# Kernel tuning notes

Measured on AMD Instinct MI355X. Metric: run time of the kernel, lower is better.

## Reference

```python
import jax, jax.numpy as jnp
import numpy as np

# AnyPrecision bit-plane packing convention (documented, since the CUDA kernel's
# exact bit order is an implementation detail):
#  - qweight[b, o, w] is an int32 word holding bit-plane b for output channel o,
#    covering input features i = 32*w .. 32*w+31, LSB-first within the word.
#  - plane 0 is the least-significant bit of the w_bits-wide LUT index.
#  - dequantized weight[o, i] = lut[o, index(o, i)].

IN_FEATURES = 4096
OUT_FEATURES = 4096
MAX_BITS = 8
W_BITS = 4


def anyprec_dequant(qweight, lut, w_bits):
    """qweight: (max_bits, O, In//32) int32; lut: (O, 2**w_bits). Returns (O, In)."""
    O, W = qweight.shape[1], qweight.shape[2]
    shifts = jnp.arange(32, dtype=jnp.int32)  # LSB-first within each word
    # (w_bits, O, W, 32): bit of each weight at each plane
    bits = (qweight[:w_bits, :, :, None] >> shifts) & 1
    plane_weights = (jnp.int32(1) << jnp.arange(w_bits, dtype=jnp.int32))[:, None, None, None]
    idx = jnp.sum(bits * plane_weights, axis=0).reshape(O, W * 32)  # (O, In) LUT indices
    return jnp.take_along_axis(lut, idx, axis=1)  # (O, In)


def setup_inputs() -> dict:
    key = jax.random.key(0)
    k1, k2, k3, k4 = jax.random.split(key, 4)
    x = jax.random.normal(k1, (4, 2048, IN_FEATURES), dtype=jnp.float32)
    qweight = jax.random.randint(
        k2, (MAX_BITS, OUT_FEATURES, IN_FEATURES // 32), 0, 2147483647, dtype=jnp.int32)
    lut = jax.random.normal(k3, (OUT_FEATURES, 2 ** W_BITS), dtype=jnp.float32) * 0.05
    bias = jax.random.normal(k4, (OUT_FEATURES,), dtype=jnp.float32) * 0.02
    return {"x": x, "qweight": qweight, "lut": lut, "bias": bias, "w_bits": W_BITS}


def reference(x, qweight, lut, bias, w_bits):
    # GEMM path of AnyPrecisionLinear.forward (B*T > 1)
    weight = anyprec_dequant(qweight, lut, w_bits)         # (O, In)
    y = jnp.einsum('bti,oi->bto', x, weight)               # (B, T, O)
    return y + bias
```

## Files before the change

kernel.cpp:

```cpp
#include <hip/hip_runtime.h>
#include <hip/hip_bf16.h>
#include <stdint.h>

#define M_DIM 8192
#define N_DIM 4096
#define K_DIM 4096

typedef __attribute__((ext_vector_type(4))) float f32x4;
typedef __attribute__((ext_vector_type(4))) int   i32x4;

#define GLD_LDS16(gaddr, laddr)                                            \
  __builtin_amdgcn_global_load_lds(                                        \
      (const __attribute__((address_space(1))) uint32_t*)(gaddr),          \
      (__attribute__((address_space(3))) uint32_t*)(laddr), 16, 0, 0)


__global__ __launch_bounds__(256) void prep_kernel(
    const int* __restrict__ q, const float* __restrict__ lut,
    signed char* __restrict__ Wq, float* __restrict__ sw,
    const float* __restrict__ x, signed char* __restrict__ Xq,
    float* __restrict__ sxd) {
  __shared__ char sm[16384];
  const int b = blockIdx.x;
  const int tid = threadIdx.x;
  if (b < 2048) {
    const int ob = b >> 4, wb = b & 15;
    const int o_l = tid >> 3, w_l = tid & 7;
    const int o = ob * 32 + o_l;
    const int PLANE = N_DIM * (K_DIM / 32);
    const int base = o * (K_DIM / 32) + wb * 8 + w_l;
    uint32_t q0 = (uint32_t)q[base];
    uint32_t q1 = (uint32_t)q[PLANE + base];
    uint32_t q2 = (uint32_t)q[2 * PLANE + base];
    uint32_t q3 = (uint32_t)q[3 * PLANE + base];
    const float* lrow = lut + o * 16;
    float lmax = 1e-30f;
#pragma unroll
    for (int j = 0; j < 16; ++j) lmax = fmaxf(lmax, fabsf(lrow[j]));
    const float qs = 127.0f / lmax;
    signed char l8[16];
#pragma unroll
    for (int j = 0; j < 16; ++j)
      l8[j] = (signed char)(int)rintf(lrow[j] * qs);
    if (wb == 0 && w_l == 0) sw[o] = lmax * (1.0f / 127.0f);

    union { i32x4 v; signed char c[16]; } u0, u1;
#pragma unroll
    for (int i = 0; i < 16; ++i) {
      uint32_t idx = ((q0 >> i) & 1u) | (((q1 >> i) & 1u) << 1) |
                     (((q2 >> i) & 1u) << 2) | (((q3 >> i) & 1u) << 3);
      u0.c[i] = l8[idx];
    }
#pragma unroll
    for (int i = 16; i < 32; ++i) {
      uint32_t idx = ((q0 >> i) & 1u) | (((q1 >> i) & 1u) << 1) |
                     (((q2 >> i) & 1u) << 2) | (((q3 >> i) & 1u) << 3);
      u1.c[i - 16] = l8[idx];
    }
    const int t_local = w_l >> 1;
    const int f_local = o_l >> 4;
    const int kc0 = (w_l & 1) * 2;
    char* sp = sm + t_local * 2048 + f_local * 1024;
    *(i32x4*)(sp + ((o_l & 15) + kc0 * 16) * 16)       = u0.v;
    *(i32x4*)(sp + ((o_l & 15) + (kc0 + 1) * 16) * 16) = u1.v;
    __syncthreads();
    const int rp = ob >> 3, h = (ob >> 2) & 1, f0 = (ob * 2) & 7;
#pragma unroll
    for (int c = 0; c < 2; ++c) {
      const int ci = c * 256 + tid;
      const int t_loc = ci >> 7, off = ci & 127;
      const size_t outb = (size_t)(rp * 64 + wb * 4 + t_loc) * 16384
                          + h * 8192 + f0 * 1024 + off * 16;
      *(i32x4*)(Wq + outb) = *(i32x4*)(sm + t_loc * 2048 + off * 16);
    }
  } else {
    const int r = b - 2048;
    const float* xr = x + (size_t)r * K_DIM;
    float v[16];
#pragma unroll
    for (int s = 0; s < 4; ++s) {
      f32x4 u = *(const f32x4*)(xr + tid * 4 + s * 1024);
      v[s * 4 + 0] = u[0]; v[s * 4 + 1] = u[1];
      v[s * 4 + 2] = u[2]; v[s * 4 + 3] = u[3];
    }
    float m = 0.0f;
#pragma unroll
    for (int i = 0; i < 16; ++i) m = fmaxf(m, fabsf(v[i]));
#pragma unroll
    for (int off = 32; off; off >>= 1) m = fmaxf(m, __shfl_down(m, off));
    float* red = (float*)(sm + 8192);
    if ((tid & 63) == 0) red[tid >> 6] = m;
    __syncthreads();
    float rmax = fmaxf(fmaxf(red[0], red[1]), fmaxf(red[2], red[3]));
    rmax = fmaxf(rmax, 1e-30f);
    if (tid == 0) sxd[r] = rmax * (1.0f / 127.0f);
    const float qs = 127.0f / rmax;
#pragma unroll
    for (int s = 0; s < 4; ++s) {
      int qi[4];
#pragma unroll
      for (int j = 0; j < 4; ++j) {
        float qc = fminf(127.0f, fmaxf(-127.0f, rintf(v[s * 4 + j] * qs)));
        qi[j] = (int)qc;
      }
      uint32_t w = (qi[0] & 255) | ((qi[1] & 255) << 8) |
                   ((qi[2] & 255) << 16) | ((uint32_t)(qi[3] & 255) << 24);
      *(uint32_t*)(sm + tid * 4 + s * 1024) = w;
    }
    __syncthreads();
    const int rp = r >> 8, h = (r >> 7) & 1, f = (r >> 4) & 7;
    const int kt = tid >> 2, kc = tid & 3;
    const size_t outb = (size_t)(rp * 64 + kt) * 16384 + h * 8192
                        + f * 1024 + ((r & 15) + kc * 16) * 16;
    *(i32x4*)(Xq + outb) = *(i32x4*)(sm + tid * 16);
  }
}

__global__ __launch_bounds__(512, 2) void anyprec_gemm_kernel(
    const signed char* __restrict__ A,
    const signed char* __restrict__ B,
    const float* __restrict__ sxd, const float* __restrict__ sw,
    const float* __restrict__ bias,
    float* __restrict__ C) {
  __shared__ char lds[2][2][2][8192];

  int bid = blockIdx.x;
  int swz = (bid & 7) * 64 + (bid >> 3);
  int mb = swz >> 4;
  int nb = swz & 15;

  const int tid  = threadIdx.x;
  const int lane = tid & 63;
  const int wid  = tid >> 6;
  const int wr   = wid >> 2;
  const int wc   = wid & 3;
  const int tid16  = tid * 16;
  const int lane16 = lane * 16;

  const char* gA = (const char*)A + (size_t)mb * 1048576;
  const char* gB = (const char*)B + (size_t)nb * 1048576;

  i32x4 acc[2][2][4][2];
#pragma unroll
  for (int qm = 0; qm < 2; ++qm)
#pragma unroll
    for (int qn = 0; qn < 2; ++qn)
#pragma unroll
      for (int mf = 0; mf < 4; ++mf)
#pragma unroll
        for (int nf = 0; nf < 2; ++nf) acc[qm][qn][mf][nf] = (i32x4)0;

  i32x4 a0[4], a1[4], b0[2], b1[2];

#define STAGE(mat, h, buf, t) {                                            \
    char* lb_ = (char*)&lds[buf][mat][h][0] + tid16;                       \
    const char* gb_ = (mat ? gB : gA) + (size_t)(t) * 16384                \
                      + (h) * 8192 + tid16;                                \
    GLD_LDS16(gb_, lb_); }

#define LDA(dst, qm, buf) {                                                \
    const char* p_ = (const char*)&lds[buf][0][qm][0] + wr * 4096          \
                     + lane16;                                             \
    _Pragma("unroll")                                                      \
    for (int mf = 0; mf < 4; ++mf)                                         \
      dst[mf] = *(const i32x4*)(p_ + mf * 1024); }

#define LDB(dst, qn, buf) {                                                \
    const char* p_ = (const char*)&lds[buf][1][qn][0] + wc * 2048          \
                     + lane16;                                             \
    _Pragma("unroll")                                                      \
    for (int nf = 0; nf < 2; ++nf)                                         \
      dst[nf] = *(const i32x4*)(p_ + nf * 1024); }

#define MMA(qm, qn, aa, bb) {                                              \
    _Pragma("unroll")                                                      \
    for (int mf = 0; mf < 4; ++mf)                                         \
      _Pragma("unroll")                                                    \
      for (int nf = 0; nf < 2; ++nf)                                       \
        acc[qm][qn][mf][nf] = __builtin_amdgcn_mfma_i32_16x16x64_i8(       \
            aa[mf], bb[nf], acc[qm][qn][mf][nf], 0, 0, 0); }

#define PRIO1 __builtin_amdgcn_s_setprio(1);
#define PRIO0 __builtin_amdgcn_s_setprio(0);
#define BAR   __builtin_amdgcn_s_barrier();
#define LGKM0 asm volatile("s_waitcnt lgkmcnt(0)" ::: "memory");
#define VMC(n) asm volatile("s_waitcnt vmcnt(" #n ")" ::: "memory");

  STAGE(0, 0, 0, 0); STAGE(1, 0, 0, 0);
  STAGE(0, 1, 0, 0); STAGE(1, 1, 0, 0);
  STAGE(0, 0, 1, 1); STAGE(1, 0, 1, 1);
  STAGE(0, 1, 1, 1); STAGE(1, 1, 1, 1);
  VMC(4); BAR;
  LDA(a0, 0, 0); LDB(b0, 0, 0); LDB(b1, 1, 0);
  LGKM0; BAR;

  for (int t = 0; t < 62; ++t) {
    const int c = t & 1, n = (t + 1) & 1;
    STAGE(0, 0, c, t + 2); STAGE(1, 0, c, t + 2);
    PRIO1; LDA(a1, 1, c); MMA(0, 0, a0, b0); MMA(0, 1, a0, b1); PRIO0;
    LGKM0; VMC(2); BAR;
    STAGE(0, 1, c, t + 2); STAGE(1, 1, c, t + 2);
    PRIO1; LDA(a0, 0, n); MMA(1, 1, a1, b1); LDB(b1, 1, n);
    MMA(1, 0, a1, b0); LDB(b0, 0, n); PRIO0;
    LGKM0; BAR;
  }

  PRIO1; LDA(a1, 1, 0); MMA(0, 0, a0, b0); MMA(0, 1, a0, b1); PRIO0;
  LGKM0; VMC(0); BAR;
  PRIO1; LDA(a0, 0, 1); MMA(1, 1, a1, b1); LDB(b1, 1, 1);
  MMA(1, 0, a1, b0); LDB(b0, 0, 1); PRIO0;
  LGKM0; BAR;
  PRIO1; LDA(a1, 1, 1); MMA(0, 0, a0, b0); MMA(0, 1, a0, b1);
  MMA(1, 1, a1, b1); MMA(1, 0, a1, b0); PRIO0;

  const int cL = lane & 15;
  const int rL = (lane >> 4) * 4;
#pragma unroll
  for (int qn = 0; qn < 2; ++qn)
#pragma unroll
    for (int nf = 0; nf < 2; ++nf) {
      int col = nb * 256 + qn * 128 + wc * 32 + nf * 16 + cL;
      float bv  = bias[col];
      float swc = sw[col];
#pragma unroll
      for (int qm = 0; qm < 2; ++qm)
#pragma unroll
        for (int mf = 0; mf < 4; ++mf) {
          int row0 = mb * 256 + qm * 128 + wr * 64 + mf * 16 + rL;
#pragma unroll
          for (int j = 0; j < 4; ++j) {
            int row = row0 + j;
            float s = sxd[row] * swc;
            C[(size_t)row * N_DIM + col] =
                fmaf((float)acc[qm][qn][mf][nf][j], s, bv);
          }
        }
    }
#undef STAGE
#undef LDA
#undef LDB
#undef MMA
#undef PRIO1
#undef PRIO0
#undef BAR
#undef LGKM0
#undef VMC
}

extern "C" void kernel_launch(void* const* d_in, const int* in_sizes, int n_in,
                              void* d_out, int out_size, void* d_ws, size_t ws_size,
                              hipStream_t stream) {
  const float* x    = (const float*)d_in[0];
  const int*   qw   = (const int*)d_in[1];
  const float* lut  = (const float*)d_in[2];
  const float* bias = (const float*)d_in[3];

  char* wsb = (char*)d_ws;
  signed char* Wq  = (signed char*)wsb;
  signed char* Xq  = (signed char*)(wsb + (size_t)16 * 1024 * 1024);
  float*       sxd = (float*)(wsb + (size_t)48 * 1024 * 1024);
  float*       sw  = sxd + M_DIM;

  {
    prep_kernel<<<10240, 256, 0, stream>>>(qw, lut, Wq, sw, x, Xq, sxd);
  }
  {
    dim3 grid((M_DIM / 256) * (N_DIM / 256));
    anyprec_gemm_kernel<<<grid, 512, 0, stream>>>(Xq, Wq, sxd, sw, bias,
                                                  (float*)d_out);
  }
}
```

Measured before the change: 193.2 us.

## Double K-tile depth to 128 and restructure GEMM into fine-grained ping-pong schedule

The packed int8 layout for weights and activations is changed so each K tile spans 128 elements instead of 64, doubling the LDS staging buffers and halving the number of main-loop tiles. The GEMM main loop is rewritten as an unrolled two-buffer schedule that interleaves per-quadrant LDS loads, global-to-LDS stages and MFMA groups separated by barriers and partial lgkmcnt waits. The aim is fewer loop iterations and barriers per unit of MFMA work and better overlap of memory with compute. In exchange it doubles LDS use to 128 KB per block, which can limit occupancy under the 2-block launch bound, and adds more barriers inside each iteration.

```diff
diff --git a/kernel.cpp b/kernel.cpp
--- a/kernel.cpp
+++ b/kernel.cpp
@@ -57,21 +57,23 @@
                      (((q2 >> i) & 1u) << 2) | (((q3 >> i) & 1u) << 3);
       u1.c[i - 16] = l8[idx];
     }
-    const int t_local = w_l >> 1;
-    const int f_local = o_l >> 4;
-    const int kc0 = (w_l & 1) * 2;
-    char* sp = sm + t_local * 2048 + f_local * 1024;
-    *(i32x4*)(sp + ((o_l & 15) + kc0 * 16) * 16)       = u0.v;
-    *(i32x4*)(sp + ((o_l & 15) + (kc0 + 1) * 16) * 16) = u1.v;
+    const int t_loc = w_l >> 2, ks = (w_l >> 1) & 1;
+    const int f_loc = o_l >> 4;
+    const int kg0 = (w_l & 1) * 2;
+    char* sp = sm + t_loc * 4096 + f_loc * 2048 + ks * 1024;
+    *(i32x4*)(sp + (((o_l & 15) + kg0 * 16)) * 16)       = u0.v;
+    *(i32x4*)(sp + (((o_l & 15) + (kg0 + 1) * 16)) * 16) = u1.v;
     __syncthreads();
-    const int rp = ob >> 3, h = (ob >> 2) & 1, f0 = (ob * 2) & 7;
+    const int rp = ob >> 3, h = (ob >> 2) & 1;
 #pragma unroll
     for (int c = 0; c < 2; ++c) {
       const int ci = c * 256 + tid;
-      const int t_loc = ci >> 7, off = ci & 127;
-      const size_t outb = (size_t)(rp * 64 + wb * 4 + t_loc) * 16384
-                          + h * 8192 + f0 * 1024 + off * 16;
-      *(i32x4*)(Wq + outb) = *(i32x4*)(sm + t_loc * 2048 + off * 16);
+      const int tl = ci >> 8, fl = (ci >> 7) & 1, ks2 = (ci >> 6) & 1,
+                l2 = ci & 63;
+      const int f = (ob * 2 + fl) & 7;
+      const size_t outb = (size_t)(rp * 32 + wb * 2 + tl) * 32768
+                          + h * 16384 + (f * 2 + ks2) * 1024 + l2 * 16;
+      *(i32x4*)(Wq + outb) = *(i32x4*)(sm + ci * 16);
     }
   } else {
     const int r = b - 2048;
@@ -109,9 +111,10 @@
     }
     __syncthreads();
     const int rp = r >> 8, h = (r >> 7) & 1, f = (r >> 4) & 7;
-    const int kt = tid >> 2, kc = tid & 3;
-    const size_t outb = (size_t)(rp * 64 + kt) * 16384 + h * 8192
-                        + f * 1024 + ((r & 15) + kc * 16) * 16;
+    const int t = tid >> 3, ks = (tid >> 2) & 1;
+    const int l = (r & 15) + (tid & 3) * 16;
+    const size_t outb = (size_t)(rp * 32 + t) * 32768 + h * 16384
+                        + (f * 2 + ks) * 1024 + l * 16;
     *(i32x4*)(Xq + outb) = *(i32x4*)(sm + tid * 16);
   }
 }
@@ -122,7 +125,7 @@
     const float* __restrict__ sxd, const float* __restrict__ sw,
     const float* __restrict__ bias,
     float* __restrict__ C) {
-  __shared__ char lds[2][2][2][8192];
+  __shared__ char lds[2][2][2][16384];
 
   int bid = blockIdx.x;
   int swz = (bid & 7) * 64 + (bid >> 3);
@@ -150,68 +153,105 @@
 #pragma unroll
         for (int nf = 0; nf < 2; ++nf) acc[qm][qn][mf][nf] = (i32x4)0;
 
-  i32x4 a0[4], a1[4], b0[2], b1[2];
+  i32x4 a0[4][2], a1[4][2], b0[2][2], b1[2][2];
 
 #define STAGE(mat, h, buf, t) {                                            \
     char* lb_ = (char*)&lds[buf][mat][h][0] + tid16;                       \
-    const char* gb_ = (mat ? gB : gA) + (size_t)(t) * 16384                \
-                      + (h) * 8192 + tid16;                                \
-    GLD_LDS16(gb_, lb_); }
+    const char* gb_ = (mat ? gB : gA) + (size_t)(t) * 32768                \
+                      + (h) * 16384 + tid16;                               \
+    GLD_LDS16(gb_,        lb_);                                            \
+    GLD_LDS16(gb_ + 8192, lb_ + 8192); }
 
 #define LDA(dst, qm, buf) {                                                \
-    const char* p_ = (const char*)&lds[buf][0][qm][0] + wr * 4096          \
+    const char* p_ = (const char*)&lds[buf][0][qm][0] + wr * 8192          \
                      + lane16;                                             \
     _Pragma("unroll")                                                      \
     for (int mf = 0; mf < 4; ++mf)                                         \
-      dst[mf] = *(const i32x4*)(p_ + mf * 1024); }
+      _Pragma("unroll")                                                    \
+      for (int ks = 0; ks < 2; ++ks)                                       \
+        dst[mf][ks] = *(const i32x4*)(p_ + mf * 2048 + ks * 1024); }
 
 #define LDB(dst, qn, buf) {                                                \
-    const char* p_ = (const char*)&lds[buf][1][qn][0] + wc * 2048          \
+    const char* p_ = (const char*)&lds[buf][1][qn][0] + wc * 4096          \
                      + lane16;                                             \
     _Pragma("unroll")                                                      \
     for (int nf = 0; nf < 2; ++nf)                                         \
-      dst[nf] = *(const i32x4*)(p_ + nf * 1024); }
+      _Pragma("unroll")                                                    \
+      for (int ks = 0; ks < 2; ++ks)                                       \
+        dst[nf][ks] = *(const i32x4*)(p_ + nf * 2048 + ks * 1024); }
 
 #define MMA(qm, qn, aa, bb) {                                              \
     _Pragma("unroll")                                                      \
     for (int mf = 0; mf < 4; ++mf)                                         \
       _Pragma("unroll")                                                    \
-      for (int nf = 0; nf < 2; ++nf)                                       \
+      for (int nf = 0; nf < 2; ++nf) {                                     \
         acc[qm][qn][mf][nf] = __builtin_amdgcn_mfma_i32_16x16x64_i8(       \
-            aa[mf], bb[nf], acc[qm][qn][mf][nf], 0, 0, 0); }
+            aa[mf][0], bb[nf][0], acc[qm][qn][mf][nf], 0, 0, 0);           \
+        acc[qm][qn][mf][nf] = __builtin_amdgcn_mfma_i32_16x16x64_i8(       \
+            aa[mf][1], bb[nf][1], acc[qm][qn][mf][nf], 0, 0, 0); } }
 
 #define PRIO1 __builtin_amdgcn_s_setprio(1);
 #define PRIO0 __builtin_amdgcn_s_setprio(0);
 #define BAR   __builtin_amdgcn_s_barrier();
 #define LGKM0 asm volatile("s_waitcnt lgkmcnt(0)" ::: "memory");
+#define LGKM8 asm volatile("s_waitcnt lgkmcnt(8)" ::: "memory");
 #define VMC(n) asm volatile("s_waitcnt vmcnt(" #n ")" ::: "memory");
 
   STAGE(0, 0, 0, 0); STAGE(1, 0, 0, 0);
   STAGE(0, 1, 0, 0); STAGE(1, 1, 0, 0);
   STAGE(0, 0, 1, 1); STAGE(1, 0, 1, 1);
-  STAGE(0, 1, 1, 1); STAGE(1, 1, 1, 1);
-  VMC(4); BAR;
-  LDA(a0, 0, 0); LDB(b0, 0, 0); LDB(b1, 1, 0);
-  LGKM0; BAR;
-
-  for (int t = 0; t < 62; ++t) {
-    const int c = t & 1, n = (t + 1) & 1;
-    STAGE(0, 0, c, t + 2); STAGE(1, 0, c, t + 2);
-    PRIO1; LDA(a1, 1, c); MMA(0, 0, a0, b0); MMA(0, 1, a0, b1); PRIO0;
-    LGKM0; VMC(2); BAR;
-    STAGE(0, 1, c, t + 2); STAGE(1, 1, c, t + 2);
-    PRIO1; LDA(a0, 0, n); MMA(1, 1, a1, b1); LDB(b1, 1, n);
-    MMA(1, 0, a1, b0); LDB(b0, 0, n); PRIO0;
-    LGKM0; BAR;
+  STAGE(1, 1, 1, 1);
+  VMC(6); BAR;
+
+  for (int i = 0; i < 15; ++i) {
+    const int O = 2 * i + 1, E2 = 2 * i + 2, O2 = 2 * i + 3;
+    LDA(a0, 0, 0); LDB(b0, 0, 0); STAGE(0, 1, 1, O);
+    LGKM8; BAR; LGKM0;
+    PRIO1; MMA(0, 0, a0, b0); PRIO0; BAR;
+    LDB(b1, 1, 0); STAGE(0, 0, 0, E2);
+    BAR; LGKM0;
+    PRIO1; MMA(0, 1, a0, b1); PRIO0; BAR;
+    LDA(a1, 1, 0); STAGE(1, 0, 0, E2);
+    BAR; LGKM0;
+    PRIO1; MMA(1, 1, a1, b1); PRIO0; BAR;
+    STAGE(1, 1, 0, E2);
+    BAR;
+    PRIO1; MMA(1, 0, a1, b0); PRIO0; VMC(6); BAR;
+    LDA(a0, 0, 1); LDB(b0, 0, 1); STAGE(0, 1, 0, E2);
+    LGKM8; BAR; LGKM0;
+    PRIO1; MMA(0, 0, a0, b0); PRIO0; BAR;
+    LDB(b1, 1, 1); STAGE(0, 0, 1, O2);
+    BAR; LGKM0;
+    PRIO1; MMA(0, 1, a0, b1); PRIO0; BAR;
+    LDA(a1, 1, 1); STAGE(1, 0, 1, O2);
+    BAR; LGKM0;
+    PRIO1; MMA(1, 1, a1, b1); PRIO0; BAR;
+    STAGE(1, 1, 1, O2);
+    BAR;
+    PRIO1; MMA(1, 0, a1, b0); PRIO0; VMC(6); BAR;
   }
 
-  PRIO1; LDA(a1, 1, 0); MMA(0, 0, a0, b0); MMA(0, 1, a0, b1); PRIO0;
-  LGKM0; VMC(0); BAR;
-  PRIO1; LDA(a0, 0, 1); MMA(1, 1, a1, b1); LDB(b1, 1, 1);
-  MMA(1, 0, a1, b0); LDB(b0, 0, 1); PRIO0;
-  LGKM0; BAR;
-  PRIO1; LDA(a1, 1, 1); MMA(0, 0, a0, b0); MMA(0, 1, a0, b1);
-  MMA(1, 1, a1, b1); MMA(1, 0, a1, b0); PRIO0;
+  LDA(a0, 0, 0); LDB(b0, 0, 0); STAGE(0, 1, 1, 31);
+  LGKM8; BAR; LGKM0;
+  PRIO1; MMA(0, 0, a0, b0); PRIO0; BAR;
+  LDB(b1, 1, 0);
+  BAR; LGKM0;
+  PRIO1; MMA(0, 1, a0, b1); PRIO0; BAR;
+  LDA(a1, 1, 0);
+  BAR; LGKM0;
+  PRIO1; MMA(1, 1, a1, b1); PRIO0; BAR;
+  BAR;
+  PRIO1; MMA(1, 0, a1, b0); PRIO0; VMC(0); BAR;
+  LDA(a0, 0, 1); LDB(b0, 0, 1);
+  LGKM8; BAR; LGKM0;
+  PRIO1; MMA(0, 0, a0, b0); PRIO0; BAR;
+  LDB(b1, 1, 1);
+  BAR; LGKM0;
+  PRIO1; MMA(0, 1, a0, b1); PRIO0; BAR;
+  LDA(a1, 1, 1);
+  BAR; LGKM0;
+  PRIO1; MMA(1, 1, a1, b1); PRIO0;
+  MMA(1, 0, a1, b0);
 
   const int cL = lane & 15;
   const int rL = (lane >> 4) * 4;
@@ -244,6 +284,7 @@
 #undef PRIO0
 #undef BAR
 #undef LGKM0
+#undef LGKM8
 #undef VMC
 }
 
```

Result: no change. 190.7 us (-1.3%).

## Restructure int8 GEMM main loop into 4-buffer, 3-deep prefetch pipeline

Applied to the files above, without the earlier changes.

Replaces the 2-buffer half-tile interleaved pipeline with a 4-slot LDS ring (128 KB total) that keeps three full k-tiles in flight. Each iteration issues the global-to-LDS loads for tile t+3, then reads all A/B fragments for the current tile and runs all MMAs, with a single barrier per tile instead of two. This is meant to hide more global-load latency and cut synchronisation overhead. In exchange it doubles LDS use, which with launch_bounds(512,2) may limit occupancy, and it loses the overlap of LDS reads with MMAs inside a tile.

```diff
diff --git a/kernel.cpp b/kernel.cpp
--- a/kernel.cpp
+++ b/kernel.cpp
@@ -122,7 +122,7 @@
     const float* __restrict__ sxd, const float* __restrict__ sw,
     const float* __restrict__ bias,
     float* __restrict__ C) {
-  __shared__ char lds[2][2][2][8192];
+  __shared__ char lds[4][32768];
 
   int bid = blockIdx.x;
   int swz = (bid & 7) * 64 + (bid >> 3);
@@ -137,6 +137,8 @@
   const int tid16  = tid * 16;
   const int lane16 = lane * 16;
 
+  char* lbase = &lds[0][0];
+
   const char* gA = (const char*)A + (size_t)mb * 1048576;
   const char* gB = (const char*)B + (size_t)nb * 1048576;
 
@@ -152,22 +154,25 @@
 
   i32x4 a0[4], a1[4], b0[2], b1[2];
 
-#define STAGE(mat, h, buf, t) {                                            \
-    char* lb_ = (char*)&lds[buf][mat][h][0] + tid16;                       \
-    const char* gb_ = (mat ? gB : gA) + (size_t)(t) * 16384                \
-                      + (h) * 8192 + tid16;                                \
-    GLD_LDS16(gb_, lb_); }
-
-#define LDA(dst, qm, buf) {                                                \
-    const char* p_ = (const char*)&lds[buf][0][qm][0] + wr * 4096          \
+#define STAGE_T(t, rb) {                                                   \
+    char* lb_ = lbase + (rb) * 32768 + tid16;                              \
+    const char* ga_ = gA + (size_t)(t) * 16384 + tid16;                    \
+    const char* gb_ = gB + (size_t)(t) * 16384 + tid16;                    \
+    GLD_LDS16(ga_,        lb_);                                            \
+    GLD_LDS16(ga_ + 8192, lb_ + 8192);                                     \
+    GLD_LDS16(gb_,        lb_ + 16384);                                    \
+    GLD_LDS16(gb_ + 8192, lb_ + 24576); }
+
+#define LDA(dst, qm, rb) {                                                 \
+    const char* p_ = lbase + (rb) * 32768 + (qm) * 8192 + wr * 4096        \
                      + lane16;                                             \
     _Pragma("unroll")                                                      \
     for (int mf = 0; mf < 4; ++mf)                                         \
       dst[mf] = *(const i32x4*)(p_ + mf * 1024); }
 
-#define LDB(dst, qn, buf) {                                                \
-    const char* p_ = (const char*)&lds[buf][1][qn][0] + wc * 2048          \
-                     + lane16;                                             \
+#define LDB(dst, qn, rb) {                                                 \
+    const char* p_ = lbase + (rb) * 32768 + 16384 + (qn) * 8192            \
+                     + wc * 2048 + lane16;                                 \
     _Pragma("unroll")                                                      \
     for (int nf = 0; nf < 2; ++nf)                                         \
       dst[nf] = *(const i32x4*)(p_ + nf * 1024); }
@@ -186,32 +191,31 @@
 #define LGKM0 asm volatile("s_waitcnt lgkmcnt(0)" ::: "memory");
 #define VMC(n) asm volatile("s_waitcnt vmcnt(" #n ")" ::: "memory");
 
-  STAGE(0, 0, 0, 0); STAGE(1, 0, 0, 0);
-  STAGE(0, 1, 0, 0); STAGE(1, 1, 0, 0);
-  STAGE(0, 0, 1, 1); STAGE(1, 0, 1, 1);
-  STAGE(0, 1, 1, 1); STAGE(1, 1, 1, 1);
-  VMC(4); BAR;
-  LDA(a0, 0, 0); LDB(b0, 0, 0); LDB(b1, 1, 0);
-  LGKM0; BAR;
-
-  for (int t = 0; t < 62; ++t) {
-    const int c = t & 1, n = (t + 1) & 1;
-    STAGE(0, 0, c, t + 2); STAGE(1, 0, c, t + 2);
-    PRIO1; LDA(a1, 1, c); MMA(0, 0, a0, b0); MMA(0, 1, a0, b1); PRIO0;
-    LGKM0; VMC(2); BAR;
-    STAGE(0, 1, c, t + 2); STAGE(1, 1, c, t + 2);
-    PRIO1; LDA(a0, 0, n); MMA(1, 1, a1, b1); LDB(b1, 1, n);
-    MMA(1, 0, a1, b0); LDB(b0, 0, n); PRIO0;
-    LGKM0; BAR;
-  }
-
-  PRIO1; LDA(a1, 1, 0); MMA(0, 0, a0, b0); MMA(0, 1, a0, b1); PRIO0;
+#define PHASE_BODY(rb)                                                     \
+    LDA(a0, 0, rb); LDB(b0, 0, rb); LDB(b1, 1, rb); LDA(a1, 1, rb);        \
+    PRIO1;                                                                 \
+    MMA(0, 0, a0, b0); MMA(0, 1, a0, b1);                                  \
+    MMA(1, 1, a1, b1); MMA(1, 0, a1, b0);                                  \
+    PRIO0;
+
+  STAGE_T(0, 0);
+  STAGE_T(1, 1);
+  STAGE_T(2, 2);
+  VMC(8); BAR;
+
+  for (int t = 0; t < 61; ++t) {
+    const int rb = t & 3;
+    STAGE_T(t + 3, (t + 3) & 3);
+    PHASE_BODY(rb);
+    LGKM0;
+    VMC(8);
+    BAR;
+  }
+  PHASE_BODY(1);
+  LGKM0; VMC(4); BAR;
+  PHASE_BODY(2);
   LGKM0; VMC(0); BAR;
-  PRIO1; LDA(a0, 0, 1); MMA(1, 1, a1, b1); LDB(b1, 1, 1);
-  MMA(1, 0, a1, b0); LDB(b0, 0, 1); PRIO0;
-  LGKM0; BAR;
-  PRIO1; LDA(a1, 1, 1); MMA(0, 0, a0, b0); MMA(0, 1, a0, b1);
-  MMA(1, 1, a1, b1); MMA(1, 0, a1, b0); PRIO0;
+  PHASE_BODY(3);
 
   const int cL = lane & 15;
   const int rL = (lane >> 4) * 4;
@@ -236,7 +240,7 @@
           }
         }
     }
-#undef STAGE
+#undef STAGE_T
 #undef LDA
 #undef LDB
 #undef MMA
@@ -245,6 +249,7 @@
 #undef BAR
 #undef LGKM0
 #undef VMC
+#undef PHASE_BODY
 }
 
 extern "C" void kernel_launch(void* const* d_in, const int* in_sizes, int n_in,
```

Result: no change. 194.7 us (+0.7%).
